# Performance work log

Measured on AMD Instinct MI355X. Metric: run time of the kernel, lower is better.

The kernel has to match this reference:

```python
import jax, jax.numpy as jnp
import numpy as np
from itertools import product

C_IN, C_OUT = 32, 64
L, T = 96, 8            # 4D grid: 96^3 spatial x 8 time
EPS = 1e-5


def _build_maps():
    """Build sparse coords and MinkowskiEngine-style kernel maps (numpy, host side)."""
    rng = np.random.default_rng(0)
    n_cand = 400000
    coords = np.stack([rng.integers(0, L, n_cand), rng.integers(0, L, n_cand),
                       rng.integers(0, L, n_cand), rng.integers(0, T, n_cand)], axis=1).astype(np.int64)
    coords = np.unique(coords, axis=0)          # [n_in, 4] unique occupied voxels
    n_in = coords.shape[0]
    # --- downsample conv: kernel_size == stride == 2 -> each input hits exactly one output
    out_coords, inv = np.unique(coords // 2, axis=0, return_inverse=True)
    n_down = out_coords.shape[0]
    off_id = ((coords[:, 0] & 1) << 3) | ((coords[:, 1] & 1) << 2) | ((coords[:, 2] & 1) << 1) | (coords[:, 3] & 1)
    g, s = [], []
    for k in range(16):
        idx = np.nonzero(off_id == k)[0]
        g.append(idx); s.append(inv[idx])
    md = max(len(a) for a in g)
    gather_d = np.full((16, md), n_in, np.int32)    # dummy -> zero pad row of input feats
    scatter_d = np.full((16, md), n_down, np.int32)  # dummy -> trash output row
    for k in range(16):
        gather_d[k, :len(g[k])] = g[k]; scatter_d[k, :len(s[k])] = s[k]
    # --- refine conv: kernel 3, stride 1 on downsampled grid (same in/out coords)
    d0, d1 = L // 2, T // 2
    def enc(c):
        return ((c[:, 0] * d0 + c[:, 1]) * d0 + c[:, 2]) * d1 + c[:, 3]
    keys = enc(out_coords)
    order = np.argsort(keys)
    skeys = keys[order]
    g, s = [], []
    for off in product((-1, 0, 1), repeat=4):
        nb = out_coords + np.asarray(off)
        ok = (nb >= 0).all(1) & (nb[:, :3] < d0).all(1) & (nb[:, 3] < d1)
        nk = enc(np.where(ok[:, None], nb, 0))
        pos = np.clip(np.searchsorted(skeys, nk), 0, n_down - 1)
        hit = ok & (skeys[pos] == nk)
        g.append(order[pos[hit]]); s.append(np.nonzero(hit)[0])
    mr = max(len(a) for a in g)
    gather_r = np.full((81, mr), n_down, np.int32)
    scatter_r = np.full((81, mr), n_down, np.int32)
    for k in range(81):
        gather_r[k, :len(g[k])] = g[k]; scatter_r[k, :len(s[k])] = s[k]
    return n_in, n_down, gather_d, scatter_d, gather_r, scatter_r


def setup_inputs() -> dict:
    n_in, n_down, gather_d, scatter_d, gather_r, scatter_r = _build_maps()
    ks = jax.random.split(jax.random.key(0), 12)
    feat = jax.random.normal(ks[0], (n_in, C_IN), jnp.float32)
    w_down = jax.random.normal(ks[1], (16, C_IN, C_OUT), jnp.float32) / np.float32(np.sqrt(16 * C_IN))
    w_ref = jax.random.normal(ks[2], (81, C_OUT, C_OUT), jnp.float32) / np.float32(np.sqrt(81 * C_OUT))
    gamma_d = jnp.abs(jax.random.normal(ks[3], (C_OUT,), jnp.float32)) + 0.5
    beta_d = jax.random.normal(ks[4], (C_OUT,), jnp.float32) * 0.1
    mean_d = jax.random.normal(ks[5], (C_OUT,), jnp.float32) * 0.1
    var_d = jax.random.uniform(ks[6], (C_OUT,), jnp.float32, 0.5, 1.5)
    gamma_r = jnp.abs(jax.random.normal(ks[7], (C_OUT,), jnp.float32)) + 0.5
    beta_r = jax.random.normal(ks[8], (C_OUT,), jnp.float32) * 0.1
    mean_r = jax.random.normal(ks[9], (C_OUT,), jnp.float32) * 0.1
    var_r = jax.random.uniform(ks[10], (C_OUT,), jnp.float32, 0.5, 1.5)
    return {"feat": feat, "w_down": w_down, "gamma_d": gamma_d, "beta_d": beta_d,
            "mean_d": mean_d, "var_d": var_d, "w_ref": w_ref, "gamma_r": gamma_r,
            "beta_r": beta_r, "mean_r": mean_r, "var_r": var_r,
            "gather_d": jnp.asarray(gather_d), "scatter_d": jnp.asarray(scatter_d),
            "gather_r": jnp.asarray(gather_r), "scatter_r": jnp.asarray(scatter_r),
            "n_down": int(n_down)}


def _spconv_bn_relu(feat, w, gather, scatter, n_out, gamma, beta, mean, var):
    # gather-GEMM-scatter sparse conv, then eval-mode BN, then ReLU
    featp = jnp.concatenate([feat, jnp.zeros((1, feat.shape[1]), feat.dtype)], axis=0)
    out = jnp.zeros((n_out + 1, w.shape[-1]), feat.dtype)
    for k in range(w.shape[0]):        # fixed small set of kernel offsets (16 or 81)
        out = out.at[scatter[k]].add(featp[gather[k]] @ w[k])
    inv = gamma * jax.lax.rsqrt(var + EPS)
    return jax.nn.relu(out[:n_out] * inv + (beta - mean * inv))


def reference(feat, w_down, gamma_d, beta_d, mean_d, var_d, w_ref, gamma_r, beta_r,
              mean_r, var_r, gather_d, scatter_d, gather_r, scatter_r, n_down):
    n_down = int(n_down)
    y = _spconv_bn_relu(feat, w_down, gather_d, scatter_d, n_down, gamma_d, beta_d, mean_d, var_d)
    y = _spconv_bn_relu(y, w_ref, gather_r, scatter_r, n_down, gamma_r, beta_r, mean_r, var_r)
    return y
```

## Files before the change

### kernel.cpp

```cpp
#include <hip/hip_runtime.h>
#include <hip/hip_bf16.h>
#include <cstdint>

#define EPS_BN 1e-5f

typedef __attribute__((ext_vector_type(8)))  short bf16x8;
typedef __attribute__((ext_vector_type(16))) float f32x16;
typedef __attribute__((ext_vector_type(4)))  unsigned short u16x4;

#define MFMA32(a, b, c) __builtin_amdgcn_mfma_f32_32x32x16_bf16(a, b, c, 0, 0, 0)

#define GLOAD_LDS16(gsrc, ldst) \
    __builtin_amdgcn_global_load_lds((const __attribute__((address_space(1))) void*)(gsrc), \
                                     (__attribute__((address_space(3))) void*)(ldst), 16, 0, 0)

__global__ void build_inv(const int* __restrict__ gather, const int* __restrict__ scatter,
                          long total, int m, int* __restrict__ invT, int n_down) {
    long i = (long)blockIdx.x * blockDim.x + threadIdx.x;
    if (i >= total) return;
    int s = scatter[i];
    if (s < n_down) {
        int k = (int)(i / m);
        invT[(long)k * n_down + s] = gather[i];
    }
}

__global__ void fcvt(const float* __restrict__ f, unsigned short* __restrict__ fb,
                     unsigned short* __restrict__ ybf_pad, long n_in) {
    long t = (long)blockIdx.x * blockDim.x + threadIdx.x;
    long e = t * 4;
    long total = n_in * 32;
    if (e < total) {
        float4 v = *(const float4*)(f + e);
        u16x4 o;
        __hip_bfloat16 h;
        h = __float2bfloat16(v.x); o.x = *(unsigned short*)&h;
        h = __float2bfloat16(v.y); o.y = *(unsigned short*)&h;
        h = __float2bfloat16(v.z); o.z = *(unsigned short*)&h;
        h = __float2bfloat16(v.w); o.w = *(unsigned short*)&h;
        *(u16x4*)(fb + e) = o;
    } else if (e < total + 32) {
        u16x4 z = {0, 0, 0, 0};
        *(u16x4*)(fb + e) = z;
    }
    if (blockIdx.x == 0 && threadIdx.x < 16) {
        u16x4 z = {0, 0, 0, 0};
        ((u16x4*)ybf_pad)[threadIdx.x] = z;
    }
}

__global__ void wcvt_r(const float* __restrict__ w, unsigned short* __restrict__ wt) {
    int e = blockIdx.x * 256 + threadIdx.x;
    int k = e >> 12, r = e & 4095;
    int cin = ((r >> 10) << 4) + (r & 15);
    int col = (r >> 4) & 63;
    __hip_bfloat16 h = __float2bfloat16(w[(k << 12) + (cin << 6) + col]);
    wt[e] = *(unsigned short*)&h;
}

__global__ void wcvt_d(const float* __restrict__ w, unsigned short* __restrict__ wt) {
    int e = blockIdx.x * 256 + threadIdx.x;
    int k = e >> 11, r = e & 2047;
    int cin = ((r >> 10) << 4) + (r & 15);
    int col = (r >> 4) & 63;
    __hip_bfloat16 h = __float2bfloat16(w[(k << 11) + (cin << 6) + col]);
    wt[e] = *(unsigned short*)&h;
}

__global__ __launch_bounds__(256, 4) void conv_down_mfma(
        const unsigned short* __restrict__ fb, const unsigned short* __restrict__ wtd,
        const int* __restrict__ invd,
        const float* __restrict__ gamma, const float* __restrict__ beta,
        const float* __restrict__ mean, const float* __restrict__ var,
        unsigned short* __restrict__ y, int n_down, int n_in) {
    int  tid  = threadIdx.x;
    int  lane = tid & 63, l31 = lane & 31, lhi = lane >> 5;
    long wv   = ((long)blockIdx.x * 256 + tid) >> 6;
    long o0   = wv * 32;
    if (o0 >= n_down) return;

    int  oA = (int)(o0 + l31 < n_down ? o0 + l31 : n_down - 1);
    bool vA = (o0 + l31) < n_down;
    const short* ysb = (const short*)fb;

#define LDI_D(k) (vA ? invd[(size_t)(k) * n_down + oA] : -1)
#define GATH_D(dst, g) { \
        const short* p = ysb + (size_t)((g) < 0 ? n_in : (g)) * 32 + lhi * 8; \
        dst[0] = *(const bf16x8*)p; dst[1] = *(const bf16x8*)(p + 16); }

    int g0 = LDI_D(0), gq1 = LDI_D(1), gq2 = LDI_D(2);
    bf16x8 ac[2];
    GATH_D(ac, g0);
    f32x16 acc0 = {}, acc1 = {};
    const short* wp = (const short*)wtd + l31 * 16 + lhi * 8;

    for (int k = 0; k < 16; ++k) {
        int gN = (k < 13) ? LDI_D(k + 3) : -1;
        bf16x8 an[2];
        GATH_D(an, gq1);
        const short* wk = wp + k * 2048;
#pragma unroll
        for (int kq = 0; kq < 2; ++kq) {
            bf16x8 b0 = *(const bf16x8*)(wk + kq * 1024);
            bf16x8 b1 = *(const bf16x8*)(wk + kq * 1024 + 512);
            acc0 = MFMA32(ac[kq], b0, acc0);
            acc1 = MFMA32(ac[kq], b1, acc1);
        }
        ac[0] = an[0]; ac[1] = an[1];
        gq1 = gq2; gq2 = gN;
    }

#pragma unroll
    for (int n = 0; n < 2; ++n) {
        int col = n * 32 + l31;
        float iv = gamma[col] * rsqrtf(var[col] + EPS_BN);
        float bb = beta[col] - mean[col] * iv;
        const f32x16& A = n ? acc1 : acc0;
#pragma unroll
        for (int i = 0; i < 16; ++i) {
            long oo = o0 + (i & 3) + 8 * (i >> 2) + 4 * lhi;
            if (oo < n_down) {
                __hip_bfloat16 h = __float2bfloat16(fmaxf(A[i] * iv + bb, 0.f));
                y[oo * 64 + col] = *(unsigned short*)&h;
            }
        }
    }
#undef LDI_D
#undef GATH_D
}

__global__ __launch_bounds__(256, 2) void conv_ref_mfma(
        const unsigned short* __restrict__ ybf, const unsigned short* __restrict__ wt,
        const int* __restrict__ invr,
        const float* __restrict__ gamma, const float* __restrict__ beta,
        const float* __restrict__ mean, const float* __restrict__ var,
        float* __restrict__ out, int n_down, int nwg) {
    __shared__ char ldsA[4][2][8192];

    int bid = blockIdx.x;
    int q = nwg >> 3, r = nwg & 7;
    int xcd = bid & 7, pos = bid >> 3;
    int swzb = (xcd < r ? xcd * (q + 1) : r * (q + 1) + (xcd - r) * q) + pos;

    const int tid  = threadIdx.x;
    const int lane = tid & 63, l31 = lane & 31, lhi = lane >> 5;
    const int wid  = tid >> 6;
    const long o0  = ((long)swzb * 4 + wid) * 64;
    if (o0 >= n_down) return;

    const int oL = (int)(o0 + lane < n_down ? o0 + lane : n_down - 1);
    const char* ybase = (const char*)ybf;
    char* ldsw = &ldsA[wid][0][0];
    const int swz = (((lane & 7) ^ (lane >> 3)) << 4);

#define STAGE(buf, gv) \
    _Pragma("unroll") \
    for (int i = 0; i < 8; ++i) { \
        int gi = __shfl((gv), (i << 3) + (lane >> 3)); \
        size_t grow = (gi < 0) ? (size_t)n_down : (size_t)gi; \
        GLOAD_LDS16(ybase + grow * 128 + swz, ldsw + (buf) * 8192 + i * 1024); \
    }

#define LDB(dst, k) { \
        const short* wk_ = wp + (size_t)(k) * 4096; \
        _Pragma("unroll") \
        for (int kq = 0; kq < 4; ++kq) { \
            dst##0[kq] = *(const bf16x8*)(wk_ + kq * 1024); \
            dst##1[kq] = *(const bf16x8*)(wk_ + kq * 1024 + 512); } }

    const int rsw = (l31 & 7) << 4;
    const int f0 = (0  + lhi * 16) ^ rsw, f1 = (32 + lhi * 16) ^ rsw;
    const int f2 = (64 + lhi * 16) ^ rsw, f3 = (96 + lhi * 16) ^ rsw;
    const int rowA = l31 * 128, rowB = (32 + l31) * 128;

#define COMPUTE(buf, B) { \
        const char* lb = ldsw + (buf) * 8192; \
        _Pragma("unroll") \
        for (int kq = 0; kq < 4; ++kq) { \
            int fo = kq == 0 ? f0 : kq == 1 ? f1 : kq == 2 ? f2 : f3; \
            bf16x8 aA = *(const bf16x8*)(lb + rowA + fo); \
            bf16x8 aB = *(const bf16x8*)(lb + rowB + fo); \
            acc0 = MFMA32(aA, B##0[kq], acc0); \
            acc1 = MFMA32(aA, B##1[kq], acc1); \
            acc2 = MFMA32(aB, B##0[kq], acc2); \
            acc3 = MFMA32(aB, B##1[kq], acc3); } }

#define WAITR { asm volatile("s_waitcnt vmcnt(17)" ::: "memory"); \
                __builtin_amdgcn_sched_barrier(0); }

    f32x16 acc0 = {}, acc1 = {}, acc2 = {}, acc3 = {};
    const short* wp = (const short*)wt + l31 * 16 + lhi * 8;
    bf16x8 Bc0[4], Bc1[4], Bn0[4], Bn1[4];

    int g0  = invr[oL];
    int gS  = invr[(size_t)n_down + oL];
    int gS2 = invr[2 * (size_t)n_down + oL];
    STAGE(0, g0);
    LDB(Bc, 0);

    for (int k = 0; k < 80; k += 2) {
        int t1, t2;
        STAGE(1, gS);
        t1 = invr[(size_t)(k + 3) * n_down + oL];
        LDB(Bn, k + 1);
        WAITR;
        COMPUTE(0, Bc);
        STAGE(0, gS2);
        t2 = invr[(size_t)(k + 4) * n_down + oL];
        LDB(Bc, k + 2);
        WAITR;
        COMPUTE(1, Bn);
        gS = t1; gS2 = t2;
    }
    asm volatile("s_waitcnt vmcnt(0)" ::: "memory");
    __builtin_amdgcn_sched_barrier(0);
    COMPUTE(0, Bc);

#pragma unroll
    for (int m = 0; m < 2; ++m)
#pragma unroll
        for (int n = 0; n < 2; ++n) {
            int col = n * 32 + l31;
            float iv = gamma[col] * rsqrtf(var[col] + EPS_BN);
            float bb = beta[col] - mean[col] * iv;
            const f32x16& A = m == 0 ? (n == 0 ? acc0 : acc1) : (n == 0 ? acc2 : acc3);
#pragma unroll
            for (int i = 0; i < 16; ++i) {
                long oo = o0 + m * 32 + (i & 3) + 8 * (i >> 2) + 4 * lhi;
                if (oo < n_down)
                    out[oo * 64 + col] = fmaxf(A[i] * iv + bb, 0.f);
            }
        }
#undef STAGE
#undef LDB
#undef COMPUTE
#undef WAITR
}

extern "C" void kernel_launch(void* const* d_in, const int* in_sizes, int n_args,
                              void* d_out, int out_size, void* d_ws, size_t ws_size,
                              hipStream_t stream) {
    const float* feat    = (const float*)d_in[0];
    const float* w_down  = (const float*)d_in[1];
    const float* gamma_d = (const float*)d_in[2];
    const float* beta_d  = (const float*)d_in[3];
    const float* mean_d  = (const float*)d_in[4];
    const float* var_d   = (const float*)d_in[5];
    const float* w_ref   = (const float*)d_in[6];
    const float* gamma_r = (const float*)d_in[7];
    const float* beta_r  = (const float*)d_in[8];
    const float* mean_r  = (const float*)d_in[9];
    const float* var_r   = (const float*)d_in[10];
    const int*   gather_d  = (const int*)d_in[11];
    const int*   scatter_d = (const int*)d_in[12];
    const int*   gather_r  = (const int*)d_in[13];
    const int*   scatter_r = (const int*)d_in[14];

    int n_in   = in_sizes[0] / 32;
    int md     = in_sizes[11] / 16;
    int mr     = in_sizes[13] / 81;
    int n_down = out_size / 64;

    char* ws = (char*)d_ws;
    size_t off = 0;
    auto alloc = [&](size_t bytes) { char* p = ws + off; off = (off + bytes + 255) & ~(size_t)255; return p; };
    unsigned short* ybf    = (unsigned short*)alloc((size_t)(n_down + 1) * 64 * 2);
    unsigned short* featbf = (unsigned short*)alloc((size_t)(n_in + 1) * 32 * 2);
    unsigned short* wt     = (unsigned short*)alloc((size_t)81 * 4096 * 2);
    unsigned short* wtd    = (unsigned short*)alloc((size_t)16 * 2048 * 2);
    int* invr = (int*)(ws + off);
    int* invd = invr + (size_t)81 * n_down;

    hipMemsetAsync(invr, 0xFF, (size_t)97 * n_down * sizeof(int), stream);

    long td = 16L * md;
    build_inv<<<(int)((td + 255) / 256), 256, 0, stream>>>(gather_d, scatter_d, td, md, invd, n_down);
    long tr = 81L * mr;
    build_inv<<<(int)((tr + 255) / 256), 256, 0, stream>>>(gather_r, scatter_r, tr, mr, invr, n_down);

    long ft = ((long)n_in * 32 + 32) / 4;
    fcvt<<<(int)((ft + 255) / 256), 256, 0, stream>>>(feat, featbf, ybf + (size_t)n_down * 64, n_in);
    wcvt_r<<<81 * 4096 / 256, 256, 0, stream>>>(w_ref, wt);
    wcvt_d<<<16 * 2048 / 256, 256, 0, stream>>>(w_down, wtd);

    long wavesD  = ((long)n_down + 31) / 32;
    int  blocksD = (int)((wavesD * 64 + 255) / 256);
    conv_down_mfma<<<blocksD, 256, 0, stream>>>(featbf, wtd, invd,
                                                gamma_d, beta_d, mean_d, var_d,
                                                ybf, n_down, n_in);

    long wavesR  = ((long)n_down + 63) / 64;
    int  blocksR = (int)((wavesR + 3) / 4);
    conv_ref_mfma<<<blocksR, 256, 0, stream>>>(ybf, wt, invr,
                                               gamma_r, beta_r, mean_r, var_r,
                                               (float*)d_out, n_down, blocksR);
}
```

Measured before the change: 392.7 us.

## Stage refine-conv weights in shared LDS per workgroup instead of per-wave registers

The refine conv kernel now has all four waves cooperatively load each 8 KB weight slice into a double-buffered shared LDS tile via global_load_lds. Each wave then reads its B fragments from LDS rather than every wave loading the full slice into registers. The weight layout is permuted to match the lane-contiguous LDS reads. The pipeline becomes one stage per offset with workgroup barriers, a deeper index prefetch and s_setprio around the MFMAs. This cuts redundant global weight traffic and register pressure, but adds two barriers per offset and drops the early exit for waves past the end, so all waves must stay in lockstep.

```diff
diff --git a/kernel.cpp b/kernel.cpp
--- a/kernel.cpp
+++ b/kernel.cpp
@@ -52,9 +52,14 @@
 __global__ void wcvt_r(const float* __restrict__ w, unsigned short* __restrict__ wt) {
     int e = blockIdx.x * 256 + threadIdx.x;
     int k = e >> 12, r = e & 4095;
-    int cin = ((r >> 10) << 4) + (r & 15);
-    int col = (r >> 4) & 63;
-    __hip_bfloat16 h = __float2bfloat16(w[(k << 12) + (cin << 6) + col]);
+    int kq  = r >> 10;
+    int n   = (r >> 9) & 1;
+    int lhi = (r >> 8) & 1;
+    int l31 = (r >> 3) & 31;
+    int j   = r & 7;
+    int cin  = (kq << 4) + (lhi << 3) + j;
+    int cout = (n << 5) + l31;
+    __hip_bfloat16 h = __float2bfloat16(w[(k << 12) + (cin << 6) + cout]);
     wt[e] = *(unsigned short*)&h;
 }
 
@@ -136,6 +141,7 @@
         const float* __restrict__ mean, const float* __restrict__ var,
         float* __restrict__ out, int n_down, int nwg) {
     __shared__ char ldsA[4][2][8192];
+    __shared__ char ldsB[2][8192];
 
     int bid = blockIdx.x;
     int q = nwg >> 3, r = nwg & 7;
@@ -146,75 +152,81 @@
     const int lane = tid & 63, l31 = lane & 31, lhi = lane >> 5;
     const int wid  = tid >> 6;
     const long o0  = ((long)swzb * 4 + wid) * 64;
-    if (o0 >= n_down) return;
 
     const int oL = (int)(o0 + lane < n_down ? o0 + lane : n_down - 1);
     const char* ybase = (const char*)ybf;
+    const char* wt_b  = (const char*)wt;
     char* ldsw = &ldsA[wid][0][0];
     const int swz = (((lane & 7) ^ (lane >> 3)) << 4);
 
-#define STAGE(buf, gv) \
+    int gi[8];
+#define BPERM(gv) \
+    _Pragma("unroll") \
+    for (int i = 0; i < 8; ++i) gi[i] = __shfl((gv), (i << 3) + (lane >> 3));
+
+#define STAGE_A(buf) \
     _Pragma("unroll") \
     for (int i = 0; i < 8; ++i) { \
-        int gi = __shfl((gv), (i << 3) + (lane >> 3)); \
-        size_t grow = (gi < 0) ? (size_t)n_down : (size_t)gi; \
-        GLOAD_LDS16(ybase + grow * 128 + swz, ldsw + (buf) * 8192 + i * 1024); \
-    }
-
-#define LDB(dst, k) { \
-        const short* wk_ = wp + (size_t)(k) * 4096; \
+        size_t grow = (size_t)(gi[i] < 0 ? n_down : gi[i]); \
+        GLOAD_LDS16(ybase + grow * 128 + swz, ldsw + (buf) * 8192 + i * 1024); }
+
+#define STAGE_B(buf, kk) { \
+        const char* src = wt_b + (size_t)(kk) * 8192 + wid * 2048; \
+        GLOAD_LDS16(src + lane * 16,        &ldsB[buf][wid * 2048]); \
+        GLOAD_LDS16(src + 1024 + lane * 16, &ldsB[buf][wid * 2048 + 1024]); }
+
+    const int rsw  = (l31 & 7) << 4;
+    const int rowA = l31 * 128, rowB = (32 + l31) * 128;
+    const int lhi16 = lhi * 16;
+
+#define COMPUTE(buf) { \
+        const char* la = ldsw + (buf) * 8192; \
+        const char* lb = &ldsB[buf][0]; \
+        __builtin_amdgcn_s_setprio(1); \
         _Pragma("unroll") \
         for (int kq = 0; kq < 4; ++kq) { \
-            dst##0[kq] = *(const bf16x8*)(wk_ + kq * 1024); \
-            dst##1[kq] = *(const bf16x8*)(wk_ + kq * 1024 + 512); } }
-
-    const int rsw = (l31 & 7) << 4;
-    const int f0 = (0  + lhi * 16) ^ rsw, f1 = (32 + lhi * 16) ^ rsw;
-    const int f2 = (64 + lhi * 16) ^ rsw, f3 = (96 + lhi * 16) ^ rsw;
-    const int rowA = l31 * 128, rowB = (32 + l31) * 128;
-
-#define COMPUTE(buf, B) { \
-        const char* lb = ldsw + (buf) * 8192; \
-        _Pragma("unroll") \
-        for (int kq = 0; kq < 4; ++kq) { \
-            int fo = kq == 0 ? f0 : kq == 1 ? f1 : kq == 2 ? f2 : f3; \
-            bf16x8 aA = *(const bf16x8*)(lb + rowA + fo); \
-            bf16x8 aB = *(const bf16x8*)(lb + rowB + fo); \
-            acc0 = MFMA32(aA, B##0[kq], acc0); \
-            acc1 = MFMA32(aA, B##1[kq], acc1); \
-            acc2 = MFMA32(aB, B##0[kq], acc2); \
-            acc3 = MFMA32(aB, B##1[kq], acc3); } }
-
-#define WAITR { asm volatile("s_waitcnt vmcnt(17)" ::: "memory"); \
-                __builtin_amdgcn_sched_barrier(0); }
+            int fo = (kq * 32 + lhi16) ^ rsw; \
+            bf16x8 aA = *(const bf16x8*)(la + rowA + fo); \
+            bf16x8 aB = *(const bf16x8*)(la + rowB + fo); \
+            bf16x8 b0 = *(const bf16x8*)(lb + kq * 2048 + lane * 16); \
+            bf16x8 b1 = *(const bf16x8*)(lb + kq * 2048 + 1024 + lane * 16); \
+            acc0 = MFMA32(aA, b0, acc0); \
+            acc1 = MFMA32(aA, b1, acc1); \
+            acc2 = MFMA32(aB, b0, acc2); \
+            acc3 = MFMA32(aB, b1, acc3); } \
+        __builtin_amdgcn_s_setprio(0); }
 
     f32x16 acc0 = {}, acc1 = {}, acc2 = {}, acc3 = {};
-    const short* wp = (const short*)wt + l31 * 16 + lhi * 8;
-    bf16x8 Bc0[4], Bc1[4], Bn0[4], Bn1[4];
-
-    int g0  = invr[oL];
-    int gS  = invr[(size_t)n_down + oL];
+
+    int ga  = invr[oL];
+    int gb  = invr[(size_t)n_down + oL];
     int gS2 = invr[2 * (size_t)n_down + oL];
-    STAGE(0, g0);
-    LDB(Bc, 0);
-
-    for (int k = 0; k < 80; k += 2) {
-        int t1, t2;
-        STAGE(1, gS);
-        t1 = invr[(size_t)(k + 3) * n_down + oL];
-        LDB(Bn, k + 1);
-        WAITR;
-        COMPUTE(0, Bc);
-        STAGE(0, gS2);
-        t2 = invr[(size_t)(k + 4) * n_down + oL];
-        LDB(Bc, k + 2);
-        WAITR;
-        COMPUTE(1, Bn);
-        gS = t1; gS2 = t2;
-    }
+    int gS3 = invr[3 * (size_t)n_down + oL];
     asm volatile("s_waitcnt vmcnt(0)" ::: "memory");
     __builtin_amdgcn_sched_barrier(0);
-    COMPUTE(0, Bc);
+    BPERM(ga);
+    STAGE_A(0);
+    STAGE_B(0, 0);
+    BPERM(gb);
+
+    for (int k = 0; k < 80; ++k) {
+        const int cur = k & 1, nxt = cur ^ 1;
+        STAGE_A(nxt);
+        STAGE_B(nxt, k + 1);
+        int gS4 = invr[(size_t)(k + 4) * n_down + oL];
+        BPERM(gS2);
+        asm volatile("s_waitcnt vmcnt(11)" ::: "memory");
+        __builtin_amdgcn_sched_barrier(0);
+        __builtin_amdgcn_s_barrier();
+        COMPUTE(cur);
+        __builtin_amdgcn_sched_barrier(0);
+        __builtin_amdgcn_s_barrier();
+        gS2 = gS3; gS3 = gS4;
+    }
+    asm volatile("s_waitcnt vmcnt(0)" ::: "memory");
+    __builtin_amdgcn_sched_barrier(0);
+    __builtin_amdgcn_s_barrier();
+    COMPUTE(0);
 
 #pragma unroll
     for (int m = 0; m < 2; ++m)
@@ -231,10 +243,10 @@
                     out[oo * 64 + col] = fmaxf(A[i] * iv + bb, 0.f);
             }
         }
-#undef STAGE
-#undef LDB
+#undef BPERM
+#undef STAGE_A
+#undef STAGE_B
 #undef COMPUTE
-#undef WAITR
 }
 
 extern "C" void kernel_launch(void* const* d_in, const int* in_sizes, int n_args,
```

Result: slower. 470.5 us (+19.8%).

## Gather refine-conv A operands directly into registers instead of LDS staging

Applied to the files above, without the earlier changes.

The refine conv kernel no longer stages gathered neighbor rows through LDS with global_load_lds and a swizzled layout. Each lane now loads its A fragments straight from global memory into registers, double-buffered, with index loads prefetched further ahead. MFMA blocks are wrapped in s_setprio to favour the matrix work. This removes the LDS traffic, the explicit vmcnt waits and the LDS allocation (which may raise occupancy), at the cost of more VGPRs and less coalesced per-lane 16-byte global loads. The downsample kernel also drops its validity check on index loads, since the index is already clamped.

```diff
diff --git a/kernel.cpp b/kernel.cpp
--- a/kernel.cpp
+++ b/kernel.cpp
@@ -9,10 +9,6 @@
 typedef __attribute__((ext_vector_type(4)))  unsigned short u16x4;
 
 #define MFMA32(a, b, c) __builtin_amdgcn_mfma_f32_32x32x16_bf16(a, b, c, 0, 0, 0)
-
-#define GLOAD_LDS16(gsrc, ldst) \
-    __builtin_amdgcn_global_load_lds((const __attribute__((address_space(1))) void*)(gsrc), \
-                                     (__attribute__((address_space(3))) void*)(ldst), 16, 0, 0)
 
 __global__ void build_inv(const int* __restrict__ gather, const int* __restrict__ scatter,
                           long total, int m, int* __restrict__ invT, int n_down) {
@@ -80,10 +76,9 @@
     if (o0 >= n_down) return;
 
     int  oA = (int)(o0 + l31 < n_down ? o0 + l31 : n_down - 1);
-    bool vA = (o0 + l31) < n_down;
     const short* ysb = (const short*)fb;
 
-#define LDI_D(k) (vA ? invd[(size_t)(k) * n_down + oA] : -1)
+#define LDI_D(k) invd[(size_t)(k) * n_down + oA]
 #define GATH_D(dst, g) { \
         const short* p = ysb + (size_t)((g) < 0 ? n_in : (g)) * 32 + lhi * 8; \
         dst[0] = *(const bf16x8*)p; dst[1] = *(const bf16x8*)(p + 16); }
@@ -135,8 +130,6 @@
         const float* __restrict__ gamma, const float* __restrict__ beta,
         const float* __restrict__ mean, const float* __restrict__ var,
         float* __restrict__ out, int n_down, int nwg) {
-    __shared__ char ldsA[4][2][8192];
-
     int bid = blockIdx.x;
     int q = nwg >> 3, r = nwg & 7;
     int xcd = bid & 7, pos = bid >> 3;
@@ -148,73 +141,67 @@
     const long o0  = ((long)swzb * 4 + wid) * 64;
     if (o0 >= n_down) return;
 
-    const int oL = (int)(o0 + lane < n_down ? o0 + lane : n_down - 1);
+    const int oLa = (int)(o0 + l31      < n_down ? o0 + l31      : n_down - 1);
+    const int oLb = (int)(o0 + 32 + l31 < n_down ? o0 + 32 + l31 : n_down - 1);
     const char* ybase = (const char*)ybf;
-    char* ldsw = &ldsA[wid][0][0];
-    const int swz = (((lane & 7) ^ (lane >> 3)) << 4);
-
-#define STAGE(buf, gv) \
-    _Pragma("unroll") \
-    for (int i = 0; i < 8; ++i) { \
-        int gi = __shfl((gv), (i << 3) + (lane >> 3)); \
-        size_t grow = (gi < 0) ? (size_t)n_down : (size_t)gi; \
-        GLOAD_LDS16(ybase + grow * 128 + swz, ldsw + (buf) * 8192 + i * 1024); \
-    }
-
-#define LDB(dst, k) { \
+
+#define LDI(k, ga, gb) { const int* p = invr + (size_t)(k) * n_down; \
+                         ga = p[oLa]; gb = p[oLb]; }
+
+#define GATH(A, ga, gb) { \
+        const char* pa_ = ybase + (size_t)((ga) < 0 ? n_down : (ga)) * 128 + lhi * 16; \
+        const char* pb_ = ybase + (size_t)((gb) < 0 ? n_down : (gb)) * 128 + lhi * 16; \
+        _Pragma("unroll") \
+        for (int kq = 0; kq < 4; ++kq) { \
+            A##a[kq] = *(const bf16x8*)(pa_ + kq * 32); \
+            A##b[kq] = *(const bf16x8*)(pb_ + kq * 32); } }
+
+#define LDB(B, k) { \
         const short* wk_ = wp + (size_t)(k) * 4096; \
         _Pragma("unroll") \
         for (int kq = 0; kq < 4; ++kq) { \
-            dst##0[kq] = *(const bf16x8*)(wk_ + kq * 1024); \
-            dst##1[kq] = *(const bf16x8*)(wk_ + kq * 1024 + 512); } }
-
-    const int rsw = (l31 & 7) << 4;
-    const int f0 = (0  + lhi * 16) ^ rsw, f1 = (32 + lhi * 16) ^ rsw;
-    const int f2 = (64 + lhi * 16) ^ rsw, f3 = (96 + lhi * 16) ^ rsw;
-    const int rowA = l31 * 128, rowB = (32 + l31) * 128;
-
-#define COMPUTE(buf, B) { \
-        const char* lb = ldsw + (buf) * 8192; \
+            B##0[kq] = *(const bf16x8*)(wk_ + kq * 1024); \
+            B##1[kq] = *(const bf16x8*)(wk_ + kq * 1024 + 512); } }
+
+#define COMPUTE(A, B) { \
+        __builtin_amdgcn_s_setprio(1); \
         _Pragma("unroll") \
         for (int kq = 0; kq < 4; ++kq) { \
-            int fo = kq == 0 ? f0 : kq == 1 ? f1 : kq == 2 ? f2 : f3; \
-            bf16x8 aA = *(const bf16x8*)(lb + rowA + fo); \
-            bf16x8 aB = *(const bf16x8*)(lb + rowB + fo); \
-            acc0 = MFMA32(aA, B##0[kq], acc0); \
-            acc1 = MFMA32(aA, B##1[kq], acc1); \
-            acc2 = MFMA32(aB, B##0[kq], acc2); \
-            acc3 = MFMA32(aB, B##1[kq], acc3); } }
-
-#define WAITR { asm volatile("s_waitcnt vmcnt(17)" ::: "memory"); \
-                __builtin_amdgcn_sched_barrier(0); }
+            acc0 = MFMA32(A##a[kq], B##0[kq], acc0); \
+            acc1 = MFMA32(A##a[kq], B##1[kq], acc1); \
+            acc2 = MFMA32(A##b[kq], B##0[kq], acc2); \
+            acc3 = MFMA32(A##b[kq], B##1[kq], acc3); } \
+        __builtin_amdgcn_s_setprio(0); }
 
     f32x16 acc0 = {}, acc1 = {}, acc2 = {}, acc3 = {};
     const short* wp = (const short*)wt + l31 * 16 + lhi * 8;
+
+    bf16x8 Aca[4], Acb[4], Ana[4], Anb[4];
     bf16x8 Bc0[4], Bc1[4], Bn0[4], Bn1[4];
 
-    int g0  = invr[oL];
-    int gS  = invr[(size_t)n_down + oL];
-    int gS2 = invr[2 * (size_t)n_down + oL];
-    STAGE(0, g0);
+    int g0a, g0b, g1a, g1b, g2a, g2b, g3a, g3b;
+    LDI(0, g0a, g0b);
+    LDI(1, g1a, g1b);
+    LDI(2, g2a, g2b);
+    LDI(3, g3a, g3b);
+    GATH(Ac, g0a, g0b);
     LDB(Bc, 0);
 
     for (int k = 0; k < 80; k += 2) {
-        int t1, t2;
-        STAGE(1, gS);
-        t1 = invr[(size_t)(k + 3) * n_down + oL];
+        int t1a, t1b, t2a, t2b;
+        GATH(An, g1a, g1b);
         LDB(Bn, k + 1);
-        WAITR;
-        COMPUTE(0, Bc);
-        STAGE(0, gS2);
-        t2 = invr[(size_t)(k + 4) * n_down + oL];
+        LDI(k + 4, t1a, t1b);
+        COMPUTE(Ac, Bc);
+        GATH(Ac, g2a, g2b);
         LDB(Bc, k + 2);
-        WAITR;
-        COMPUTE(1, Bn);
-        gS = t1; gS2 = t2;
-    }
-    asm volatile("s_waitcnt vmcnt(0)" ::: "memory");
-    __builtin_amdgcn_sched_barrier(0);
-    COMPUTE(0, Bc);
+        if (k < 76) { LDI(k + 5, t2a, t2b); } else { t2a = -1; t2b = -1; }
+        COMPUTE(An, Bn);
+        g1a = g3a; g1b = g3b;
+        g2a = t1a; g2b = t1b;
+        g3a = t2a; g3b = t2b;
+    }
+    COMPUTE(Ac, Bc);
 
 #pragma unroll
     for (int m = 0; m < 2; ++m)
@@ -231,10 +218,10 @@
                     out[oo * 64 + col] = fmaxf(A[i] * iv + bb, 0.f);
             }
         }
-#undef STAGE
+#undef LDI
+#undef GATH
 #undef LDB
 #undef COMPUTE
-#undef WAITR
 }
 
 extern "C" void kernel_launch(void* const* d_in, const int* in_sizes, int n_args,
```

New measurement: 517.9 us. 31.9% more time.

## Halve refine-conv wave tile to 32 rows for higher occupancy

Applied to the files above, without the earlier changes.

Each wave of the refine conv now computes 32 output rows instead of 64. This halves the accumulators and LDS staging and raises launch bounds to 3 blocks per CU. Each lane now loads its gather indices directly rather than shuffling them, and the MFMA section is wrapped in s_setprio. The down conv drops its validity check on index loads, relying on the clamp. The cost is that weight (B) fragments are reused across half as many rows, so weight traffic per output doubles.

```diff
diff --git a/kernel.cpp b/kernel.cpp
--- a/kernel.cpp
+++ b/kernel.cpp
@@ -80,10 +80,9 @@
     if (o0 >= n_down) return;
 
     int  oA = (int)(o0 + l31 < n_down ? o0 + l31 : n_down - 1);
-    bool vA = (o0 + l31) < n_down;
     const short* ysb = (const short*)fb;
 
-#define LDI_D(k) (vA ? invd[(size_t)(k) * n_down + oA] : -1)
+#define LDI_D(k) invd[(size_t)(k) * n_down + oA]
 #define GATH_D(dst, g) { \
         const short* p = ysb + (size_t)((g) < 0 ? n_in : (g)) * 32 + lhi * 8; \
         dst[0] = *(const bf16x8*)p; dst[1] = *(const bf16x8*)(p + 16); }
@@ -129,13 +128,13 @@
 #undef GATH_D
 }
 
-__global__ __launch_bounds__(256, 2) void conv_ref_mfma(
+__global__ __launch_bounds__(256, 3) void conv_ref_mfma(
         const unsigned short* __restrict__ ybf, const unsigned short* __restrict__ wt,
         const int* __restrict__ invr,
         const float* __restrict__ gamma, const float* __restrict__ beta,
         const float* __restrict__ mean, const float* __restrict__ var,
         float* __restrict__ out, int n_down, int nwg) {
-    __shared__ char ldsA[4][2][8192];
+    __shared__ char ldsA[4][2][4096];
 
     int bid = blockIdx.x;
     int q = nwg >> 3, r = nwg & 7;
@@ -145,92 +144,104 @@
     const int tid  = threadIdx.x;
     const int lane = tid & 63, l31 = lane & 31, lhi = lane >> 5;
     const int wid  = tid >> 6;
-    const long o0  = ((long)swzb * 4 + wid) * 64;
+    const long o0  = ((long)swzb * 4 + wid) * 32;
     if (o0 >= n_down) return;
 
-    const int oL = (int)(o0 + lane < n_down ? o0 + lane : n_down - 1);
     const char* ybase = (const char*)ybf;
     char* ldsw = &ldsA[wid][0][0];
-    const int swz = (((lane & 7) ^ (lane >> 3)) << 4);
-
-#define STAGE(buf, gv) \
-    _Pragma("unroll") \
-    for (int i = 0; i < 8; ++i) { \
-        int gi = __shfl((gv), (i << 3) + (lane >> 3)); \
-        size_t grow = (gi < 0) ? (size_t)n_down : (size_t)gi; \
-        GLOAD_LDS16(ybase + grow * 128 + swz, ldsw + (buf) * 8192 + i * 1024); \
-    }
-
-#define LDB(dst, k) { \
+    const int ro  = lane >> 3;
+    const int swz = (((lane & 7) ^ ro) << 4);
+
+    int oI0 = (int)(o0 + 0  + ro < n_down ? o0 + 0  + ro : n_down - 1);
+    int oI1 = (int)(o0 + 8  + ro < n_down ? o0 + 8  + ro : n_down - 1);
+    int oI2 = (int)(o0 + 16 + ro < n_down ? o0 + 16 + ro : n_down - 1);
+    int oI3 = (int)(o0 + 24 + ro < n_down ? o0 + 24 + ro : n_down - 1);
+
+#define LDI(k, Q) { const int* p_ = invr + (size_t)(k) * n_down; \
+        Q##0 = p_[oI0]; Q##1 = p_[oI1]; Q##2 = p_[oI2]; Q##3 = p_[oI3]; }
+
+#define STAGE(buf, Q) { \
+        size_t r0_ = (size_t)(Q##0 < 0 ? n_down : Q##0); \
+        size_t r1_ = (size_t)(Q##1 < 0 ? n_down : Q##1); \
+        size_t r2_ = (size_t)(Q##2 < 0 ? n_down : Q##2); \
+        size_t r3_ = (size_t)(Q##3 < 0 ? n_down : Q##3); \
+        GLOAD_LDS16(ybase + r0_ * 128 + swz, ldsw + (buf) * 4096); \
+        GLOAD_LDS16(ybase + r1_ * 128 + swz, ldsw + (buf) * 4096 + 1024); \
+        GLOAD_LDS16(ybase + r2_ * 128 + swz, ldsw + (buf) * 4096 + 2048); \
+        GLOAD_LDS16(ybase + r3_ * 128 + swz, ldsw + (buf) * 4096 + 3072); }
+
+#define LDB(B, k) { \
         const short* wk_ = wp + (size_t)(k) * 4096; \
         _Pragma("unroll") \
         for (int kq = 0; kq < 4; ++kq) { \
-            dst##0[kq] = *(const bf16x8*)(wk_ + kq * 1024); \
-            dst##1[kq] = *(const bf16x8*)(wk_ + kq * 1024 + 512); } }
-
-    const int rsw = (l31 & 7) << 4;
-    const int f0 = (0  + lhi * 16) ^ rsw, f1 = (32 + lhi * 16) ^ rsw;
-    const int f2 = (64 + lhi * 16) ^ rsw, f3 = (96 + lhi * 16) ^ rsw;
-    const int rowA = l31 * 128, rowB = (32 + l31) * 128;
+            B##0[kq] = *(const bf16x8*)(wk_ + kq * 1024); \
+            B##1[kq] = *(const bf16x8*)(wk_ + kq * 1024 + 512); } }
+
+    const int rsw   = (l31 & 7) << 4;
+    const int rowA  = l31 * 128;
+    const int lhi16 = lhi * 16;
 
 #define COMPUTE(buf, B) { \
-        const char* lb = ldsw + (buf) * 8192; \
+        const char* la = ldsw + (buf) * 4096; \
+        __builtin_amdgcn_s_setprio(1); \
         _Pragma("unroll") \
         for (int kq = 0; kq < 4; ++kq) { \
-            int fo = kq == 0 ? f0 : kq == 1 ? f1 : kq == 2 ? f2 : f3; \
-            bf16x8 aA = *(const bf16x8*)(lb + rowA + fo); \
-            bf16x8 aB = *(const bf16x8*)(lb + rowB + fo); \
-            acc0 = MFMA32(aA, B##0[kq], acc0); \
-            acc1 = MFMA32(aA, B##1[kq], acc1); \
-            acc2 = MFMA32(aB, B##0[kq], acc2); \
-            acc3 = MFMA32(aB, B##1[kq], acc3); } }
-
-#define WAITR { asm volatile("s_waitcnt vmcnt(17)" ::: "memory"); \
+            int fo = (kq * 32 + lhi16) ^ rsw; \
+            bf16x8 a_ = *(const bf16x8*)(la + rowA + fo); \
+            acc0 = MFMA32(a_, B##0[kq], acc0); \
+            acc1 = MFMA32(a_, B##1[kq], acc1); } \
+        __builtin_amdgcn_s_setprio(0); }
+
+#define WAITR { asm volatile("s_waitcnt vmcnt(16)" ::: "memory"); \
                 __builtin_amdgcn_sched_barrier(0); }
 
-    f32x16 acc0 = {}, acc1 = {}, acc2 = {}, acc3 = {};
+    f32x16 acc0 = {}, acc1 = {};
     const short* wp = (const short*)wt + l31 * 16 + lhi * 8;
     bf16x8 Bc0[4], Bc1[4], Bn0[4], Bn1[4];
-
-    int g0  = invr[oL];
-    int gS  = invr[(size_t)n_down + oL];
-    int gS2 = invr[2 * (size_t)n_down + oL];
-    STAGE(0, g0);
+    int qA0, qA1, qA2, qA3;
+    int qB0, qB1, qB2, qB3;
+    int t0, t1, t2, t3, u0, u1, u2, u3;
+
+    LDI(0, t);
+    LDI(1, qA);
+    LDI(2, qB);
+    asm volatile("s_waitcnt vmcnt(8)" ::: "memory");
+    __builtin_amdgcn_sched_barrier(0);
+    STAGE(0, t);
     LDB(Bc, 0);
 
     for (int k = 0; k < 80; k += 2) {
-        int t1, t2;
-        STAGE(1, gS);
-        t1 = invr[(size_t)(k + 3) * n_down + oL];
+        LDI(k + 3, t);
+        STAGE(1, qA);
         LDB(Bn, k + 1);
         WAITR;
         COMPUTE(0, Bc);
-        STAGE(0, gS2);
-        t2 = invr[(size_t)(k + 4) * n_down + oL];
+        LDI(k + 4, u);
+        STAGE(0, qB);
         LDB(Bc, k + 2);
         WAITR;
         COMPUTE(1, Bn);
-        gS = t1; gS2 = t2;
+        qA0 = t0; qA1 = t1; qA2 = t2; qA3 = t3;
+        qB0 = u0; qB1 = u1; qB2 = u2; qB3 = u3;
     }
     asm volatile("s_waitcnt vmcnt(0)" ::: "memory");
     __builtin_amdgcn_sched_barrier(0);
     COMPUTE(0, Bc);
 
 #pragma unroll
-    for (int m = 0; m < 2; ++m)
-#pragma unroll
-        for (int n = 0; n < 2; ++n) {
-            int col = n * 32 + l31;
-            float iv = gamma[col] * rsqrtf(var[col] + EPS_BN);
-            float bb = beta[col] - mean[col] * iv;
-            const f32x16& A = m == 0 ? (n == 0 ? acc0 : acc1) : (n == 0 ? acc2 : acc3);
-#pragma unroll
-            for (int i = 0; i < 16; ++i) {
-                long oo = o0 + m * 32 + (i & 3) + 8 * (i >> 2) + 4 * lhi;
-                if (oo < n_down)
-                    out[oo * 64 + col] = fmaxf(A[i] * iv + bb, 0.f);
-            }
+    for (int n = 0; n < 2; ++n) {
+        int col = n * 32 + l31;
+        float iv = gamma[col] * rsqrtf(var[col] + EPS_BN);
+        float bb = beta[col] - mean[col] * iv;
+        const f32x16& A = n == 0 ? acc0 : acc1;
+#pragma unroll
+        for (int i = 0; i < 16; ++i) {
+            long oo = o0 + (i & 3) + 8 * (i >> 2) + 4 * lhi;
+            if (oo < n_down)
+                out[oo * 64 + col] = fmaxf(A[i] * iv + bb, 0.f);
         }
+    }
+#undef LDI
 #undef STAGE
 #undef LDB
 #undef COMPUTE
@@ -289,8 +300,7 @@
                                                 gamma_d, beta_d, mean_d, var_d,
                                                 ybf, n_down, n_in);
 
-    long wavesR  = ((long)n_down + 63) / 64;
-    int  blocksR = (int)((wavesR + 3) / 4);
+    int blocksR = (n_down + 127) / 128;
     conv_ref_mfma<<<blocksR, 256, 0, stream>>>(ybf, wt, invr,
                                                gamma_r, beta_r, mean_r, var_r,
                                                (float*)d_out, n_down, blocksR);
```

Result: slower. 463.0 us (+17.9%).
